# Optimization experiments

Hardware: AMD Instinct MI355X
Metric: run time of the kernel (lower is better)

The kernel has to match this reference:

```python
import jax, jax.numpy as jnp
import numpy as np

N = 50000
E = 600000
D_IN = 128
D_OUT = 128
EPS = 1e-12  # F.normalize eps


def setup_inputs() -> dict:
    key = jax.random.key(0)
    ks = jax.random.split(key, 10)
    s = 1.0 / np.sqrt(D_IN)
    inp = {
        "x": jax.random.normal(ks[0], (N, D_IN), dtype=jnp.float32),
        "edge_index": jax.random.randint(ks[1], (2, E), 0, N, dtype=jnp.int64),
        # conv1: lin_l (with bias) applied to aggregated neighbors, lin_r (no bias) to root
        "W1l": jax.random.uniform(ks[2], (D_IN, D_IN), jnp.float32, -s, s),
        "b1": jax.random.uniform(ks[3], (D_IN,), jnp.float32, -s, s),
        "W1r": jax.random.uniform(ks[4], (D_IN, D_IN), jnp.float32, -s, s),
        # conv2
        "W2l": jax.random.uniform(ks[5], (D_IN, D_OUT), jnp.float32, -s, s),
        "b2": jax.random.uniform(ks[6], (D_OUT,), jnp.float32, -s, s),
        "W2r": jax.random.uniform(ks[7], (D_IN, D_OUT), jnp.float32, -s, s),
        # final fc
        "Wf": jax.random.uniform(ks[8], (D_OUT, D_OUT), jnp.float32, -s, s),
        "bf": jax.random.uniform(ks[9], (D_OUT,), jnp.float32, -s, s),
    }
    return inp


def _sage_conv(x, src, dst, Wl, bl, Wr):
    # mean-aggregate messages from source nodes onto destination nodes
    msgs = x[src]  # [E, d] gather
    agg = jax.ops.segment_sum(msgs, dst, num_segments=N)  # [N, d]
    cnt = jax.ops.segment_sum(jnp.ones((src.shape[0],), x.dtype), dst, num_segments=N)
    agg = agg / jnp.maximum(cnt, 1.0)[:, None]  # isolated nodes -> 0
    out = agg @ Wl + bl + x @ Wr
    # L2 normalize per node (PyG normalize=True)
    nrm = jnp.sqrt(jnp.sum(out * out, axis=-1, keepdims=True))
    return out / jnp.maximum(nrm, EPS)


def reference(x, edge_index, W1l, b1, W1r, W2l, b2, W2r, Wf, bf):
    src, dst = edge_index[0], edge_index[1]
    h = jax.nn.relu(_sage_conv(x, src, dst, W1l, b1, W1r))
    h = jax.nn.relu(_sage_conv(h, src, dst, W2l, b2, W2r))
    return h @ Wf + bf
```

## Files before the change

kernel.cpp:

```cpp
#include <hip/hip_runtime.h>
#include <hip/hip_fp16.h>

#define D 128
#define SCAN_B 256
#define HLD 136

typedef __attribute__((ext_vector_type(8))) _Float16 f16x8;
typedef __attribute__((ext_vector_type(4))) float f32x4;

__global__ void scan_pass1(const int* __restrict__ cnt, int* __restrict__ rs,
                           int* __restrict__ bsum, int N) {
    __shared__ int lds[SCAN_B];
    int tid = threadIdx.x;
    int i = blockIdx.x * SCAN_B + tid;
    int v = (i < N) ? cnt[i] : 0;
    lds[tid] = v;
    __syncthreads();
    for (int o = 1; o < SCAN_B; o <<= 1) {
        int t = (tid >= o) ? lds[tid - o] : 0;
        __syncthreads();
        lds[tid] += t;
        __syncthreads();
    }
    if (i < N) rs[i] = lds[tid] - v;
    if (tid == SCAN_B - 1) bsum[blockIdx.x] = lds[tid];
}

__global__ void scan_pass2(int* __restrict__ bsum, int nb) {
    __shared__ int lds[SCAN_B];
    int tid = threadIdx.x;
    int v = (tid < nb) ? bsum[tid] : 0;
    lds[tid] = v;
    __syncthreads();
    for (int o = 1; o < SCAN_B; o <<= 1) {
        int t = (tid >= o) ? lds[tid - o] : 0;
        __syncthreads();
        lds[tid] += t;
        __syncthreads();
    }
    if (tid < nb) bsum[tid] = lds[tid] - v;
}

__global__ void scan_pass3(int* __restrict__ rs, int* __restrict__ cursor,
                           const int* __restrict__ bsum, const int* __restrict__ cnt,
                           float* __restrict__ inv, int N) {
    int i = blockIdx.x * SCAN_B + threadIdx.x;
    if (i < N) {
        int v = rs[i] + bsum[blockIdx.x];
        rs[i] = v;
        cursor[i] = v;
        inv[i] = 1.0f / (float)max(cnt[i], 1);
    }
}

__global__ void fill_kernel(const int* __restrict__ ei, int E,
                            int* __restrict__ cursor, int* __restrict__ csr) {
    int e = blockIdx.x * blockDim.x + threadIdx.x;
    if (e < E) {
        int src = ei[e], dst = ei[E + e];
        int pos = atomicAdd(&cursor[dst], 1);
        csr[pos] = src;
    }
}

__global__ void prologue_kernel(const float* __restrict__ W1l, const float* __restrict__ W1r,
                                const float* __restrict__ W2l, const float* __restrict__ W2r,
                                const float* __restrict__ Wf, unsigned short* __restrict__ pw,
                                const float* __restrict__ x, __half* __restrict__ xh, int n8,
                                const int* __restrict__ ei, int E, int* __restrict__ cnt) {
    int t = blockIdx.x * blockDim.x + threadIdx.x;
    if (t < 10240) {
        int idx = t;
        int w = idx >> 11;
        int r = idx & 2047;
        int ks = r >> 9;
        int tt = (r >> 6) & 7;
        int lane = r & 63;
        int q = lane >> 4, n = lane & 15;
        const float* W = (w == 0) ? W1l : (w == 1) ? W1r : (w == 2) ? W2l : (w == 3) ? W2r : Wf;
        unsigned short* dh = pw + (size_t)w * 32768;
        unsigned short* dl = dh + 16384;
        int off = ((ks * 8 + tt) * 64 + lane) * 8;
#pragma unroll
        for (int j = 0; j < 8; j++) {
            float v = W[(size_t)(ks * 32 + q * 8 + j) * D + tt * 16 + n];
            __half hb = __float2half_rn(v);
            dh[off + j] = __half_as_ushort(hb);
            dl[off + j] = __half_as_ushort(__float2half_rn(v - __half2float(hb)));
        }
    } else if (t < 10240 + n8) {
        int i = t - 10240;
        const float4* x4 = (const float4*)x;
        float4 a = x4[2 * i], b = x4[2 * i + 1];
        __half2 h0 = __floats2half2_rn(a.x, a.y);
        __half2 h1 = __floats2half2_rn(a.z, a.w);
        __half2 h2 = __floats2half2_rn(b.x, b.y);
        __half2 h3 = __floats2half2_rn(b.z, b.w);
        uint4 o;
        o.x = *(const unsigned*)&h0;
        o.y = *(const unsigned*)&h1;
        o.z = *(const unsigned*)&h2;
        o.w = *(const unsigned*)&h3;
        ((uint4*)xh)[i] = o;
    } else {
        int e = t - 10240 - n8;
        if (e < E) atomicAdd(&cnt[ei[E + e]], 1);
    }
}

__device__ __forceinline__ void acc8(uint4 v, float* s) {
    const __half2* h = reinterpret_cast<const __half2*>(&v);
    float2 f0 = __half22float2(h[0]);
    float2 f1 = __half22float2(h[1]);
    float2 f2 = __half22float2(h[2]);
    float2 f3 = __half22float2(h[3]);
    s[0] += f0.x; s[1] += f0.y; s[2] += f1.x; s[3] += f1.y;
    s[4] += f2.x; s[5] += f2.y; s[6] += f3.x; s[7] += f3.y;
}

__global__ void aggregate_kernel(const __half* __restrict__ xh, int sstride,
                                 const int* __restrict__ csr,
                                 const int* __restrict__ rs, const int* __restrict__ cnt,
                                 const float* __restrict__ inv,
                                 __half* __restrict__ aggh, __half* __restrict__ aggl, int N) {
    int t = blockIdx.x * blockDim.x + threadIdx.x;
    int node = t >> 4;
    int c = t & 15;
    if (node >= N) return;
    int deg = cnt[node];
    int st = rs[node];
    const uint4* x4 = (const uint4*)xh;
    float s[8] = {0.f, 0.f, 0.f, 0.f, 0.f, 0.f, 0.f, 0.f};
    int i = 0;
    for (; i + 4 <= deg; i += 4) {
        int n0 = csr[st + i + 0], n1 = csr[st + i + 1];
        int n2 = csr[st + i + 2], n3 = csr[st + i + 3];
        uint4 v0 = x4[(size_t)n0 * sstride + c];
        uint4 v1 = x4[(size_t)n1 * sstride + c];
        uint4 v2 = x4[(size_t)n2 * sstride + c];
        uint4 v3 = x4[(size_t)n3 * sstride + c];
        acc8(v0, s); acc8(v1, s); acc8(v2, s); acc8(v3, s);
    }
    for (; i < deg; i++) {
        int n0 = csr[st + i];
        uint4 v0 = x4[(size_t)n0 * sstride + c];
        acc8(v0, s);
    }
    float iv = inv[node];
    uint4 oh, ol;
    __half2* ph = (__half2*)&oh;
    __half2* pl = (__half2*)&ol;
#pragma unroll
    for (int jj = 0; jj < 4; jj++) {
        float v0 = s[2 * jj] * iv, v1 = s[2 * jj + 1] * iv;
        __half h0 = __float2half_rn(v0), h1 = __float2half_rn(v1);
        ph[jj] = __halves2half2(h0, h1);
        pl[jj] = __halves2half2(__float2half_rn(v0 - __half2float(h0)),
                                __float2half_rn(v1 - __half2float(h1)));
    }
    ((uint4*)aggh)[(size_t)node * 16 + c] = oh;
    ((uint4*)aggl)[(size_t)node * 16 + c] = ol;
}

__device__ __forceinline__ void split_f16(const float* v, uint4& hi, uint4& lo) {
    __half2* ph = (__half2*)&hi;
    __half2* pl = (__half2*)&lo;
#pragma unroll
    for (int jj = 0; jj < 4; jj++) {
        __half h0 = __float2half_rn(v[2 * jj]);
        __half h1 = __float2half_rn(v[2 * jj + 1]);
        ph[jj] = __halves2half2(h0, h1);
        pl[jj] = __halves2half2(__float2half_rn(v[2 * jj] - __half2float(h0)),
                                __float2half_rn(v[2 * jj + 1] - __half2float(h1)));
    }
}

__device__ __forceinline__ void w_issue(const uint4* __restrict__ srch,
                                        const uint4* __restrict__ srcl,
                                        int wave, int lane, uint4* st) {
    const uint4* src = ((wave < 2) ? srch : srcl) + ((wave & 1) * 256 + lane);
#pragma unroll
    for (int i = 0; i < 4; i++) st[i] = src[i * 64];
}
__device__ __forceinline__ void w_commit(char* dstbase, int wave, int lane, const uint4* st) {
    uint4* dst = (uint4*)(dstbase + wave * 4096 + lane * 16);
#pragma unroll
    for (int i = 0; i < 4; i++) dst[i * 64] = st[i];
}

template <int LAYER>
__global__ __launch_bounds__(256) void mfma_gemm(
        const uint4* __restrict__ Agh, const uint4* __restrict__ Agl,
        const float* __restrict__ Xf,
        const uint4* Hio,
        const uint4* __restrict__ W0h, const uint4* __restrict__ W0l,
        const uint4* __restrict__ W1h, const uint4* __restrict__ W1l,
        const float* __restrict__ bias,
        const uint4* __restrict__ W2h, const uint4* __restrict__ W2l,
        const float* __restrict__ bias2,
        float* out, __half* Hout, int N) {
    __shared__ uint4 smem4[(LAYER == 2 ? 51200 : 32768) / 16];
    char* smem = (char*)smem4;

    const int tid = threadIdx.x;
    const int lane = tid & 63;
    const int wave = tid >> 6;
    const int c = lane & 15;
    const int q = lane >> 4;
    const int R = blockIdx.x * 64 + wave * 16;
    const int row0 = min(R + c, N - 1);
    const size_t rb16 = (size_t)row0 * 16 + q;

    auto wsrc_h = [&](int ks) { return ((ks < 4) ? W0h : W1h) + (size_t)(ks & 3) * 512; };
    auto wsrc_l = [&](int ks) { return ((ks < 4) ? W0l : W1l) + (size_t)(ks & 3) * 512; };
    auto load_a = [&](int ks, uint4& ah, uint4& al) {
        if (ks < 4) {
            ah = Agh[rb16 + ks * 4];
            al = Agl[rb16 + ks * 4];
        } else if (LAYER == 1) {
            const float4* xf4 = (const float4*)Xf;
            size_t xb = (size_t)row0 * 32 + q * 2 + (size_t)(ks - 4) * 8;
            float4 xa = xf4[xb], xb2 = xf4[xb + 1];
            float v[8] = {xa.x, xa.y, xa.z, xa.w, xb2.x, xb2.y, xb2.z, xb2.w};
            split_f16(v, ah, al);
        } else {
            size_t rb32 = (size_t)row0 * 32 + q + (size_t)(ks - 4) * 4;
            ah = Hio[rb32];
            al = Hio[rb32 + 16];
        }
    };

    uint4 st[4];
    uint4 A_h[2], A_l[2];
    w_issue(wsrc_h(0), wsrc_l(0), wave, lane, st);
    load_a(0, A_h[0], A_l[0]);
    w_commit(smem, wave, lane, st);
    __syncthreads();

    f32x4 acc[8];
#pragma unroll
    for (int t = 0; t < 8; t++)
#pragma unroll
        for (int r = 0; r < 4; r++) acc[t][r] = 0.0f;

#pragma unroll
    for (int ks = 0; ks < 8; ks++) {
        const int b = ks & 1;
        if (ks < 7) {
            w_issue(wsrc_h(ks + 1), wsrc_l(ks + 1), wave, lane, st);
            load_a(ks + 1, A_h[b ^ 1], A_l[b ^ 1]);
        }
        const uint4* wb = (const uint4*)(smem + b * 16384);
        f16x8 ah = __builtin_bit_cast(f16x8, A_h[b]);
        f16x8 al = __builtin_bit_cast(f16x8, A_l[b]);
#pragma unroll
        for (int t = 0; t < 8; t++) {
            f16x8 bh = __builtin_bit_cast(f16x8, wb[t * 64 + lane]);
            f16x8 bl = __builtin_bit_cast(f16x8, wb[512 + t * 64 + lane]);
            acc[t] = __builtin_amdgcn_mfma_f32_16x16x32_f16(ah, bh, acc[t], 0, 0, 0);
            acc[t] = __builtin_amdgcn_mfma_f32_16x16x32_f16(al, bh, acc[t], 0, 0, 0);
            acc[t] = __builtin_amdgcn_mfma_f32_16x16x32_f16(ah, bl, acc[t], 0, 0, 0);
        }
        if (ks < 7) w_commit(smem + (b ^ 1) * 16384, wave, lane, st);
        __syncthreads();
    }

#pragma unroll
    for (int t = 0; t < 8; t++) {
        float bv = bias[t * 16 + c];
#pragma unroll
        for (int r = 0; r < 4; r++) acc[t][r] += bv;
    }
#pragma unroll
    for (int r = 0; r < 4; r++) {
        float v = 0.0f;
#pragma unroll
        for (int t = 0; t < 8; t++) v += acc[t][r] * acc[t][r];
        v += __shfl_xor(v, 1, 16);
        v += __shfl_xor(v, 2, 16);
        v += __shfl_xor(v, 4, 16);
        v += __shfl_xor(v, 8, 16);
        float rn = 1.0f / fmaxf(sqrtf(v), 1e-12f);
#pragma unroll
        for (int t = 0; t < 8; t++) acc[t][r] = fmaxf(acc[t][r] * rn, 0.0f);
    }

    if (LAYER == 1) {
#pragma unroll
        for (int t = 0; t < 8; t++)
#pragma unroll
            for (int r = 0; r < 4; r++) {
                int row = R + q * 4 + r;
                if (row < N) {
                    float v = acc[t][r];
                    __half h = __float2half_rn(v);
                    size_t base = (size_t)row * 256;
                    Hout[base + t * 16 + c] = h;
                    Hout[base + 128 + t * 16 + c] = __float2half_rn(v - __half2float(h));
                }
            }
        return;
    }

    uint4 stf[4];
    w_issue(W2h, W2l, wave, lane, stf);

    __half* hh = (__half*)smem + wave * (2 * 16 * HLD);
    __half* hl = hh + 16 * HLD;
#pragma unroll
    for (int t = 0; t < 8; t++)
#pragma unroll
        for (int r = 0; r < 4; r++) {
            int m = q * 4 + r;
            float v = acc[t][r];
            __half h = __float2half_rn(v);
            hh[m * HLD + t * 16 + c] = h;
            hl[m * HLD + t * 16 + c] = __float2half_rn(v - __half2float(h));
        }
    char* wfb = smem + 34816;
    w_commit(wfb, wave, lane, stf);
    __syncthreads();

    uint4 a2h_[4], a2l_[4];
#pragma unroll
    for (int k2 = 0; k2 < 4; k2++) {
        a2h_[k2] = *(const uint4*)&hh[c * HLD + k2 * 32 + q * 8];
        a2l_[k2] = *(const uint4*)&hl[c * HLD + k2 * 32 + q * 8];
    }

    f32x4 acc2[8];
#pragma unroll
    for (int t = 0; t < 8; t++) {
        float bv = bias2[t * 16 + c];
#pragma unroll
        for (int r = 0; r < 4; r++) acc2[t][r] = bv;
    }
    const uint4* wb2 = (const uint4*)wfb;
#pragma unroll
    for (int k2 = 0; k2 < 4; k2++) {
        if (k2 < 3) w_issue(W2h + (size_t)(k2 + 1) * 512, W2l + (size_t)(k2 + 1) * 512,
                            wave, lane, stf);
        f16x8 ah = __builtin_bit_cast(f16x8, a2h_[k2]);
        f16x8 al = __builtin_bit_cast(f16x8, a2l_[k2]);
#pragma unroll
        for (int t = 0; t < 8; t++) {
            f16x8 bh = __builtin_bit_cast(f16x8, wb2[t * 64 + lane]);
            f16x8 bl = __builtin_bit_cast(f16x8, wb2[512 + t * 64 + lane]);
            acc2[t] = __builtin_amdgcn_mfma_f32_16x16x32_f16(ah, bh, acc2[t], 0, 0, 0);
            acc2[t] = __builtin_amdgcn_mfma_f32_16x16x32_f16(al, bh, acc2[t], 0, 0, 0);
            acc2[t] = __builtin_amdgcn_mfma_f32_16x16x32_f16(ah, bl, acc2[t], 0, 0, 0);
        }
        if (k2 < 3) {
            __syncthreads();
            w_commit(wfb, wave, lane, stf);
            __syncthreads();
        }
    }

#pragma unroll
    for (int t = 0; t < 8; t++)
#pragma unroll
        for (int r = 0; r < 4; r++) {
            int row = R + q * 4 + r;
            if (row < N) out[(size_t)row * D + t * 16 + c] = acc2[t][r];
        }
}

extern "C" void kernel_launch(void* const* d_in, const int* in_sizes, int n_in,
                              void* d_out, int out_size, void* d_ws, size_t ws_size,
                              hipStream_t stream) {
    const float* x   = (const float*)d_in[0];
    const int*   ei  = (const int*)d_in[1];
    const float* W1l = (const float*)d_in[2];
    const float* b1  = (const float*)d_in[3];
    const float* W1r = (const float*)d_in[4];
    const float* W2l = (const float*)d_in[5];
    const float* b2  = (const float*)d_in[6];
    const float* W2r = (const float*)d_in[7];
    const float* Wf  = (const float*)d_in[8];
    const float* bf  = (const float*)d_in[9];
    float* out = (float*)d_out;

    int N = in_sizes[0] / D;
    int E = in_sizes[1] / 2;

    __half* Agh = (__half*)d_ws;
    __half* Agl = Agh + (size_t)N * D;
    __half* Xh  = Agl + (size_t)N * D;
    float* inv  = (float*)(Xh + (size_t)N * D);
    int*   rs     = (int*)(inv + N);
    int*   cnt    = rs + N;
    int*   cursor = cnt + N;
    int*   bsum   = cursor + N;
    int*   csr    = bsum + 256;
    unsigned short* pw = (unsigned short*)(csr + E);
    unsigned short* p1lh = pw + 0 * 32768, *p1ll = p1lh + 16384;
    unsigned short* p1rh = pw + 1 * 32768, *p1rl = p1rh + 16384;
    unsigned short* p2lh = pw + 2 * 32768, *p2ll = p2lh + 16384;
    unsigned short* p2rh = pw + 3 * 32768, *p2rl = p2rh + 16384;
    unsigned short* pfh  = pw + 4 * 32768, *pfl  = pfh + 16384;

    __half* H1 = (__half*)d_out;

    int nb = (N + SCAN_B - 1) / SCAN_B;
    int n8 = N * 16;

    hipMemsetAsync(cnt, 0, (size_t)N * sizeof(int), stream);
    int pro_threads = 10240 + n8 + E;
    prologue_kernel<<<(pro_threads + 255) / 256, 256, 0, stream>>>(
        W1l, W1r, W2l, W2r, Wf, pw, x, Xh, n8, ei, E, cnt);
    scan_pass1<<<nb, SCAN_B, 0, stream>>>(cnt, rs, bsum, N);
    scan_pass2<<<1, SCAN_B, 0, stream>>>(bsum, nb);
    scan_pass3<<<nb, SCAN_B, 0, stream>>>(rs, cursor, bsum, cnt, inv, N);
    fill_kernel<<<(E + 255) / 256, 256, 0, stream>>>(ei, E, cursor, csr);

    int agg_blocks = (N * 16 + 255) / 256;
    int gemm_blocks = (N + 63) / 64;

    aggregate_kernel<<<agg_blocks, 256, 0, stream>>>(Xh, 16, csr, rs, cnt, inv, Agh, Agl, N);
    mfma_gemm<1><<<gemm_blocks, 256, 0, stream>>>(
        (const uint4*)Agh, (const uint4*)Agl, x, nullptr,
        (const uint4*)p1lh, (const uint4*)p1ll, (const uint4*)p1rh, (const uint4*)p1rl, b1,
        nullptr, nullptr, nullptr, nullptr, H1, N);

    aggregate_kernel<<<agg_blocks, 256, 0, stream>>>(H1, 32, csr, rs, cnt, inv, Agh, Agl, N);
    mfma_gemm<2><<<gemm_blocks, 256, 0, stream>>>(
        (const uint4*)Agh, (const uint4*)Agl, nullptr, (const uint4*)d_out,
        (const uint4*)p2lh, (const uint4*)p2ll, (const uint4*)p2rh, (const uint4*)p2rl, b2,
        (const uint4*)pfh, (const uint4*)pfl, bf, out, nullptr, N);
}
```

Measured before the change: 310.3 us.

## Stage GEMM weights via direct global-to-LDS loads and shrink shared memory

Replaces register-staged weight copies with global_load_lds direct-to-LDS transfers double-buffered two steps ahead, and shrinks shared memory from 32-50 KB to 32 KB. Layer-1 root input is pre-split into fp16 hi/lo in the prologue instead of splitting fp32 in the GEMM. The final fc layer reads weights straight from global memory instead of LDS and uses an XOR-swizzled LDS tile for the hidden activations. This aims to cut register pressure, LDS traffic and barriers, and to raise occupancy. In exchange it adds an extra fp16 buffer write in the prologue, more global reads for the fc weights, and waitcnt(0) stalls.

```diff
diff --git a/kernel.cpp b/kernel.cpp
--- a/kernel.cpp
+++ b/kernel.cpp
@@ -3,10 +3,12 @@
 
 #define D 128
 #define SCAN_B 256
-#define HLD 136
 
 typedef __attribute__((ext_vector_type(8))) _Float16 f16x8;
 typedef __attribute__((ext_vector_type(4))) float f32x4;
+
+typedef __attribute__((address_space(1))) const void gas_t;
+typedef __attribute__((address_space(3))) void las_t;
 
 __global__ void scan_pass1(const int* __restrict__ cnt, int* __restrict__ rs,
                            int* __restrict__ bsum, int N) {
@@ -66,7 +68,8 @@
 __global__ void prologue_kernel(const float* __restrict__ W1l, const float* __restrict__ W1r,
                                 const float* __restrict__ W2l, const float* __restrict__ W2r,
                                 const float* __restrict__ Wf, unsigned short* __restrict__ pw,
-                                const float* __restrict__ x, __half* __restrict__ xh, int n8,
+                                const float* __restrict__ x, __half* __restrict__ xh,
+                                __half* __restrict__ xl, int n8,
                                 const int* __restrict__ ei, int E, int* __restrict__ cnt) {
     int t = blockIdx.x * blockDim.x + threadIdx.x;
     if (t < 10240) {
@@ -92,16 +95,20 @@
         int i = t - 10240;
         const float4* x4 = (const float4*)x;
         float4 a = x4[2 * i], b = x4[2 * i + 1];
-        __half2 h0 = __floats2half2_rn(a.x, a.y);
-        __half2 h1 = __floats2half2_rn(a.z, a.w);
-        __half2 h2 = __floats2half2_rn(b.x, b.y);
-        __half2 h3 = __floats2half2_rn(b.z, b.w);
-        uint4 o;
-        o.x = *(const unsigned*)&h0;
-        o.y = *(const unsigned*)&h1;
-        o.z = *(const unsigned*)&h2;
-        o.w = *(const unsigned*)&h3;
-        ((uint4*)xh)[i] = o;
+        float v[8] = {a.x, a.y, a.z, a.w, b.x, b.y, b.z, b.w};
+        uint4 oh, ol;
+        __half2* ph = (__half2*)&oh;
+        __half2* pl = (__half2*)&ol;
+#pragma unroll
+        for (int jj = 0; jj < 4; jj++) {
+            __half h0 = __float2half_rn(v[2 * jj]);
+            __half h1 = __float2half_rn(v[2 * jj + 1]);
+            ph[jj] = __halves2half2(h0, h1);
+            pl[jj] = __halves2half2(__float2half_rn(v[2 * jj] - __half2float(h0)),
+                                    __float2half_rn(v[2 * jj + 1] - __half2float(h1)));
+        }
+        ((uint4*)xh)[i] = oh;
+        ((uint4*)xl)[i] = ol;
     } else {
         int e = t - 10240 - n8;
         if (e < E) atomicAdd(&cnt[ei[E + e]], 1);
@@ -162,45 +169,17 @@
     ((uint4*)aggl)[(size_t)node * 16 + c] = ol;
 }
 
-__device__ __forceinline__ void split_f16(const float* v, uint4& hi, uint4& lo) {
-    __half2* ph = (__half2*)&hi;
-    __half2* pl = (__half2*)&lo;
-#pragma unroll
-    for (int jj = 0; jj < 4; jj++) {
-        __half h0 = __float2half_rn(v[2 * jj]);
-        __half h1 = __float2half_rn(v[2 * jj + 1]);
-        ph[jj] = __halves2half2(h0, h1);
-        pl[jj] = __halves2half2(__float2half_rn(v[2 * jj] - __half2float(h0)),
-                                __float2half_rn(v[2 * jj + 1] - __half2float(h1)));
-    }
-}
-
-__device__ __forceinline__ void w_issue(const uint4* __restrict__ srch,
-                                        const uint4* __restrict__ srcl,
-                                        int wave, int lane, uint4* st) {
-    const uint4* src = ((wave < 2) ? srch : srcl) + ((wave & 1) * 256 + lane);
-#pragma unroll
-    for (int i = 0; i < 4; i++) st[i] = src[i * 64];
-}
-__device__ __forceinline__ void w_commit(char* dstbase, int wave, int lane, const uint4* st) {
-    uint4* dst = (uint4*)(dstbase + wave * 4096 + lane * 16);
-#pragma unroll
-    for (int i = 0; i < 4; i++) dst[i * 64] = st[i];
-}
-
 template <int LAYER>
 __global__ __launch_bounds__(256) void mfma_gemm(
         const uint4* __restrict__ Agh, const uint4* __restrict__ Agl,
-        const float* __restrict__ Xf,
-        const uint4* Hio,
+        const uint4* __restrict__ Ah1, const uint4* __restrict__ Al1,
         const uint4* __restrict__ W0h, const uint4* __restrict__ W0l,
         const uint4* __restrict__ W1h, const uint4* __restrict__ W1l,
         const float* __restrict__ bias,
         const uint4* __restrict__ W2h, const uint4* __restrict__ W2l,
         const float* __restrict__ bias2,
         float* out, __half* Hout, int N) {
-    __shared__ uint4 smem4[(LAYER == 2 ? 51200 : 32768) / 16];
-    char* smem = (char*)smem4;
+    __shared__ uint4 smem4[2048];
 
     const int tid = threadIdx.x;
     const int lane = tid & 63;
@@ -210,31 +189,37 @@
     const int R = blockIdx.x * 64 + wave * 16;
     const int row0 = min(R + c, N - 1);
     const size_t rb16 = (size_t)row0 * 16 + q;
-
-    auto wsrc_h = [&](int ks) { return ((ks < 4) ? W0h : W1h) + (size_t)(ks & 3) * 512; };
-    auto wsrc_l = [&](int ks) { return ((ks < 4) ? W0l : W1l) + (size_t)(ks & 3) * 512; };
-    auto load_a = [&](int ks, uint4& ah, uint4& al) {
-        if (ks < 4) {
-            ah = Agh[rb16 + ks * 4];
-            al = Agl[rb16 + ks * 4];
-        } else if (LAYER == 1) {
-            const float4* xf4 = (const float4*)Xf;
-            size_t xb = (size_t)row0 * 32 + q * 2 + (size_t)(ks - 4) * 8;
-            float4 xa = xf4[xb], xb2 = xf4[xb + 1];
-            float v[8] = {xa.x, xa.y, xa.z, xa.w, xb2.x, xb2.y, xb2.z, xb2.w};
-            split_f16(v, ah, al);
-        } else {
-            size_t rb32 = (size_t)row0 * 32 + q + (size_t)(ks - 4) * 4;
-            ah = Hio[rb32];
-            al = Hio[rb32 + 16];
-        }
-    };
-
-    uint4 st[4];
+    const size_t rbA1 = (size_t)row0 * (LAYER == 1 ? 16 : 32) + q;
+
+#define STAGE_W(ks_, b_)                                                                   \
+    do {                                                                                   \
+        const uint4* sh_ = (((ks_) < 4) ? W0h : W1h) + (size_t)((ks_) & 3) * 512;          \
+        const uint4* sl_ = (((ks_) < 4) ? W0l : W1l) + (size_t)((ks_) & 3) * 512;          \
+        const uint4* s_ = ((wave < 2) ? sh_ : sl_) + ((wave & 1) * 256 + lane);            \
+        uint4* d_ = smem4 + (b_) * 1024 + (wave >> 1) * 512 + (wave & 1) * 256;            \
+        __builtin_amdgcn_global_load_lds((gas_t*)(s_), (las_t*)(d_), 16, 0, 0);            \
+        __builtin_amdgcn_global_load_lds((gas_t*)(s_ + 64), (las_t*)(d_ + 64), 16, 0, 0);  \
+        __builtin_amdgcn_global_load_lds((gas_t*)(s_ + 128), (las_t*)(d_ + 128), 16, 0, 0);\
+        __builtin_amdgcn_global_load_lds((gas_t*)(s_ + 192), (las_t*)(d_ + 192), 16, 0, 0);\
+    } while (0)
+
+#define LOAD_A(ks_, s_)                                                       \
+    do {                                                                      \
+        if ((ks_) < 4) {                                                      \
+            A_h[s_] = Agh[rb16 + (ks_) * 4];                                  \
+            A_l[s_] = Agl[rb16 + (ks_) * 4];                                  \
+        } else {                                                              \
+            A_h[s_] = Ah1[rbA1 + ((ks_) - 4) * 4];                            \
+            A_l[s_] = Al1[rbA1 + ((ks_) - 4) * 4];                            \
+        }                                                                     \
+    } while (0)
+
     uint4 A_h[2], A_l[2];
-    w_issue(wsrc_h(0), wsrc_l(0), wave, lane, st);
-    load_a(0, A_h[0], A_l[0]);
-    w_commit(smem, wave, lane, st);
+    STAGE_W(0, 0);
+    STAGE_W(1, 1);
+    LOAD_A(0, 0);
+    LOAD_A(1, 1);
+    asm volatile("s_waitcnt vmcnt(0)" ::: "memory");
     __syncthreads();
 
     f32x4 acc[8];
@@ -246,11 +231,7 @@
 #pragma unroll
     for (int ks = 0; ks < 8; ks++) {
         const int b = ks & 1;
-        if (ks < 7) {
-            w_issue(wsrc_h(ks + 1), wsrc_l(ks + 1), wave, lane, st);
-            load_a(ks + 1, A_h[b ^ 1], A_l[b ^ 1]);
-        }
-        const uint4* wb = (const uint4*)(smem + b * 16384);
+        const uint4* wb = smem4 + b * 1024;
         f16x8 ah = __builtin_bit_cast(f16x8, A_h[b]);
         f16x8 al = __builtin_bit_cast(f16x8, A_l[b]);
 #pragma unroll
@@ -261,8 +242,14 @@
             acc[t] = __builtin_amdgcn_mfma_f32_16x16x32_f16(al, bh, acc[t], 0, 0, 0);
             acc[t] = __builtin_amdgcn_mfma_f32_16x16x32_f16(ah, bl, acc[t], 0, 0, 0);
         }
-        if (ks < 7) w_commit(smem + (b ^ 1) * 16384, wave, lane, st);
-        __syncthreads();
+        if (ks < 7) {
+            asm volatile("s_waitcnt vmcnt(0)" ::: "memory");
+            __syncthreads();
+            if (ks < 6) {
+                STAGE_W(ks + 2, b);
+                LOAD_A(ks + 2, b);
+            }
+        }
     }
 
 #pragma unroll
@@ -302,11 +289,8 @@
         return;
     }
 
-    uint4 stf[4];
-    w_issue(W2h, W2l, wave, lane, stf);
-
-    __half* hh = (__half*)smem + wave * (2 * 16 * HLD);
-    __half* hl = hh + 16 * HLD;
+    __syncthreads();
+    unsigned short* hw = (unsigned short*)(smem4 + wave * 512);
 #pragma unroll
     for (int t = 0; t < 8; t++)
 #pragma unroll
@@ -314,18 +298,17 @@
             int m = q * 4 + r;
             float v = acc[t][r];
             __half h = __float2half_rn(v);
-            hh[m * HLD + t * 16 + c] = h;
-            hl[m * HLD + t * 16 + c] = __float2half_rn(v - __half2float(h));
-        }
-    char* wfb = smem + 34816;
-    w_commit(wfb, wave, lane, stf);
-    __syncthreads();
-
+            int j4 = (t * 2 + (c >> 3)) ^ (m & 7);
+            int off = m * 128 + j4 * 8 + (c & 7);
+            hw[off] = __half_as_ushort(h);
+            hw[2048 + off] = __half_as_ushort(__float2half_rn(v - __half2float(h)));
+        }
     uint4 a2h_[4], a2l_[4];
 #pragma unroll
     for (int k2 = 0; k2 < 4; k2++) {
-        a2h_[k2] = *(const uint4*)&hh[c * HLD + k2 * 32 + q * 8];
-        a2l_[k2] = *(const uint4*)&hl[c * HLD + k2 * 32 + q * 8];
+        int r4 = (k2 * 4 + q) ^ (c & 7);
+        a2h_[k2] = *(const uint4*)(hw + c * 128 + r4 * 8);
+        a2l_[k2] = *(const uint4*)(hw + 2048 + c * 128 + r4 * 8);
     }
 
     f32x4 acc2[8];
@@ -335,26 +318,20 @@
 #pragma unroll
         for (int r = 0; r < 4; r++) acc2[t][r] = bv;
     }
-    const uint4* wb2 = (const uint4*)wfb;
 #pragma unroll
     for (int k2 = 0; k2 < 4; k2++) {
-        if (k2 < 3) w_issue(W2h + (size_t)(k2 + 1) * 512, W2l + (size_t)(k2 + 1) * 512,
-                            wave, lane, stf);
+        const uint4* Wh = W2h + (size_t)k2 * 512 + lane;
+        const uint4* Wl = W2l + (size_t)k2 * 512 + lane;
         f16x8 ah = __builtin_bit_cast(f16x8, a2h_[k2]);
         f16x8 al = __builtin_bit_cast(f16x8, a2l_[k2]);
 #pragma unroll
         for (int t = 0; t < 8; t++) {
-            f16x8 bh = __builtin_bit_cast(f16x8, wb2[t * 64 + lane]);
-            f16x8 bl = __builtin_bit_cast(f16x8, wb2[512 + t * 64 + lane]);
+            f16x8 bh = __builtin_bit_cast(f16x8, Wh[t * 64]);
+            f16x8 bl = __builtin_bit_cast(f16x8, Wl[t * 64]);
             acc2[t] = __builtin_amdgcn_mfma_f32_16x16x32_f16(ah, bh, acc2[t], 0, 0, 0);
             acc2[t] = __builtin_amdgcn_mfma_f32_16x16x32_f16(al, bh, acc2[t], 0, 0, 0);
             acc2[t] = __builtin_amdgcn_mfma_f32_16x16x32_f16(ah, bl, acc2[t], 0, 0, 0);
         }
-        if (k2 < 3) {
-            __syncthreads();
-            w_commit(wfb, wave, lane, stf);
-            __syncthreads();
-        }
     }
 
 #pragma unroll
@@ -364,6 +341,8 @@
             int row = R + q * 4 + r;
             if (row < N) out[(size_t)row * D + t * 16 + c] = acc2[t][r];
         }
+#undef STAGE_W
+#undef LOAD_A
 }
 
 extern "C" void kernel_launch(void* const* d_in, const int* in_sizes, int n_in,
@@ -387,7 +366,8 @@
     __half* Agh = (__half*)d_ws;
     __half* Agl = Agh + (size_t)N * D;
     __half* Xh  = Agl + (size_t)N * D;
-    float* inv  = (float*)(Xh + (size_t)N * D);
+    __half* Xl  = Xh + (size_t)N * D;
+    float* inv  = (float*)(Xl + (size_t)N * D);
     int*   rs     = (int*)(inv + N);
     int*   cnt    = rs + N;
     int*   cursor = cnt + N;
@@ -408,7 +388,7 @@
     hipMemsetAsync(cnt, 0, (size_t)N * sizeof(int), stream);
     int pro_threads = 10240 + n8 + E;
     prologue_kernel<<<(pro_threads + 255) / 256, 256, 0, stream>>>(
-        W1l, W1r, W2l, W2r, Wf, pw, x, Xh, n8, ei, E, cnt);
+        W1l, W1r, W2l, W2r, Wf, pw, x, Xh, Xl, n8, ei, E, cnt);
     scan_pass1<<<nb, SCAN_B, 0, stream>>>(cnt, rs, bsum, N);
     scan_pass2<<<1, SCAN_B, 0, stream>>>(bsum, nb);
     scan_pass3<<<nb, SCAN_B, 0, stream>>>(rs, cursor, bsum, cnt, inv, N);
@@ -419,13 +399,14 @@
 
     aggregate_kernel<<<agg_blocks, 256, 0, stream>>>(Xh, 16, csr, rs, cnt, inv, Agh, Agl, N);
     mfma_gemm<1><<<gemm_blocks, 256, 0, stream>>>(
-        (const uint4*)Agh, (const uint4*)Agl, x, nullptr,
+        (const uint4*)Agh, (const uint4*)Agl, (const uint4*)Xh, (const uint4*)Xl,
         (const uint4*)p1lh, (const uint4*)p1ll, (const uint4*)p1rh, (const uint4*)p1rl, b1,
         nullptr, nullptr, nullptr, nullptr, H1, N);
 
     aggregate_kernel<<<agg_blocks, 256, 0, stream>>>(H1, 32, csr, rs, cnt, inv, Agh, Agl, N);
     mfma_gemm<2><<<gemm_blocks, 256, 0, stream>>>(
-        (const uint4*)Agh, (const uint4*)Agl, nullptr, (const uint4*)d_out,
+        (const uint4*)Agh, (const uint4*)Agl,
+        (const uint4*)d_out, (const uint4*)d_out + 16,
         (const uint4*)p2lh, (const uint4*)p2ll, (const uint4*)p2rh, (const uint4*)p2rl, b2,
         (const uint4*)pfh, (const uint4*)pfl, bf, out, nullptr, N);
 }
```

New measurement: 261.0 us. 1.19x faster.
